# Kernel tuning notes

Hardware: AMD Instinct MI355X
Metric: run time of the kernel (lower is better)

The kernel has to match this reference:

```python
import jax, jax.numpy as jnp
import numpy as np

N_SAMPLES = 32768
SAMPLES_PER_FRAME = 256
N_FRAMES = N_SAMPLES // SAMPLES_PER_FRAME  # 128
SAMPLERATE = 22050
NYQUIST = SAMPLERATE // 2
MIN_FREQ = 40.0 / NYQUIST
MAX_FREQ = 4000.0 / NYQUIST
FREQ_SCALE = MAX_FREQ - MIN_FREQ
TWO_PI = 2.0 * np.pi


def lin_interp(x, out_size):
    """torch F.interpolate(mode='linear', align_corners=False) along last axis."""
    in_size = x.shape[-1]
    scale = in_size / out_size
    coords = (jnp.arange(out_size, dtype=x.dtype) + 0.5) * scale - 0.5
    coords = jnp.clip(coords, 0.0, in_size - 1)
    i0 = jnp.floor(coords).astype(jnp.int32)
    i1 = jnp.minimum(i0 + 1, in_size - 1)
    w = coords - i0.astype(x.dtype)
    return x[..., i0] * (1.0 - w) + x[..., i1] * w


def setup_inputs() -> dict:
    key = jax.random.key(0)
    k1, k2 = jax.random.split(key)
    f0 = jax.random.uniform(k1, (4, 16, 1), dtype=jnp.float32)  # normalized freq in [0,1)
    # resonance decay factors, realistic range near [0.75, 0.999)
    res = 0.75 + 0.249 * jax.random.uniform(k2, (4, 16, 32), dtype=jnp.float32)
    factors = jnp.arange(1, 33, dtype=jnp.float32)  # harmonic multipliers 1..32
    return {"f0": f0, "res": res, "factors": factors}


def reference(f0, res, factors):
    B, E, _ = f0.shape
    F_ = factors.shape[0]
    # map f0 in [0,1] to normalized frequency band
    f0 = MIN_FREQ + FREQ_SCALE * f0                      # (B, E, 1)
    freqs = f0 * factors[None, None, :]                  # (B, E, F)
    freqs = jnp.where(freqs >= 1.0, 0.0, freqs)          # zero out aliased harmonics
    # repeat per frame then upsample to sample rate
    freqs = jnp.broadcast_to(freqs[..., None], (B, E, F_, N_FRAMES))
    freqs = lin_interp(freqs, N_SAMPLES)                 # (B, E, F, N_SAMPLES)
    # exponential decay envelope: cumprod over frames via exp(cumsum(log))
    log_res = jnp.log(res + 1e-12)                       # (B, E, F)
    log_env = jnp.cumsum(
        jnp.broadcast_to(log_res[..., None], (B, E, F_, N_FRAMES)), axis=-1)
    env = jnp.exp(log_env)
    env = lin_interp(env, N_SAMPLES)                     # (B, E, F, N_SAMPLES)
    # integrate phase and oscillate
    phase = jnp.cumsum(freqs * TWO_PI, axis=-1)
    final = env * jnp.sin(phase)                         # (B, E, F, N_SAMPLES)
    return jnp.sum(final, axis=2)                        # (B, E, N_SAMPLES)
```

## Files before the change

### kernel.cpp

```cpp
#include <hip/hip_runtime.h>
#include <hip/hip_bf16.h>


#define NSAMP 32768
#define NFRM  128
#define NF    32
#define NP2   (NF / 2)
#define NPAIR 64
#define CHUNKS 16
#define CHUNK (NSAMP / CHUNKS)
#define KIT   (CHUNK / 256)

typedef __attribute__((ext_vector_type(2))) float f32x2;

__device__ __forceinline__ f32x2 pk_fma(f32x2 a, f32x2 b, f32x2 c) {
    return __builtin_elementwise_fma(a, b, c);
}

__device__ __forceinline__ float ldin(const void* p, int i, bool isbf) {
    if (isbf) {
        unsigned int w = ((unsigned int)((const unsigned short*)p)[i]) << 16;
        float f; __builtin_memcpy(&f, &w, 4); return f;
    }
    return ((const float*)p)[i];
}

__device__ __forceinline__ float rfl(float x) {
    int i; __builtin_memcpy(&i, &x, 4);
    i = __builtin_amdgcn_readfirstlane(i);
    float f; __builtin_memcpy(&f, &i, 4); return f;
}

extern "C" __global__ __launch_bounds__(256, 4)
void reson_kernel(const void* __restrict__ f0p,
                  const void* __restrict__ resp,
                  const void* __restrict__ facp,
                  void* __restrict__ outp)
{
    const bool isbf = (((const unsigned int*)facp)[0] != 0x3F800000u);

    const int pair = blockIdx.x;
    const int y    = blockIdx.y;
    const int tid  = threadIdx.x;
    const int n0   = y * CHUNK + tid;

    const float MINF = (float)(40.0 / 11025.0);
    const float FSC  = (float)(3960.0 / 11025.0);

    __shared__ __align__(16) float sR[NF];
    __shared__ __align__(16) float sP[NF];

    const float f0v = rfl(ldin(f0p, pair, isbf));
    const float sf0 = MINF + FSC * f0v;
    const unsigned int Q1 = (unsigned int)((double)sf0 * 4294967296.0 + 0.5);

    if (tid < NF) {
        const float r   = ldin(resp, pair * NF + tid, isbf);
        const float fac = ldin(facp, tid, isbf);
        float P = exp2f(log2f(r) * (float)(8 * y));
        if (sf0 * fac >= 1.0f) P = 0.0f;
        sR[tid] = r;
        sP[tid] = P;
    }
    __syncthreads();

    const float c0raw = (n0 + 0.5f) * (1.0f / 256.0f) - 0.5f;
    const bool useR1 = (tid >= 128) || (y == 0);

    f32x2 E[NP2];
    f32x2 Rv[NP2];
    #pragma unroll
    for (int j = 0; j < NP2; ++j) {
        const f32x2 p2 = *(const f32x2*)&sP[2 * j];
        const f32x2 r2 = *(const f32x2*)&sR[2 * j];
        Rv[j].x = rfl(r2.x); Rv[j].y = rfl(r2.y);
        E[j] = useR1 ? (f32x2)(p2 * Rv[j]) : p2;
    }

    const int obase = pair * NSAMP + n0;

    if (y != 0 && y != CHUNKS - 1) {
        const float w0 = c0raw - floorf(c0raw);
        const f32x2 w0v = {w0, w0};
        #pragma unroll
        for (int j = 0; j < NP2; ++j) {
            const f32x2 M = E[j];
            E[j] = pk_fma(w0v, pk_fma(M, Rv[j], -M), M);
        }
        #pragma unroll 1
        for (int k = 0; k < KIT; ++k) {
            const unsigned int nn = (unsigned int)(n0 + (k << 8) + 1);
            const unsigned int qn = Q1 * nn;
            const float t1 = (float)qn * 0x1p-32f;
            const float t2 = (float)(qn << 1) * 0x1p-32f;
            const float s1 = __builtin_amdgcn_sinf(t1);
            const float s2 = __builtin_amdgcn_sinf(t2);
            const float c2 = __builtin_amdgcn_cosf(t2);
            const float k2s = c2 + c2;
            const f32x2 k2 = {k2s, k2s};
            f32x2 sp = {-s1, 0.0f};
            f32x2 sc = {s1, s2};
            f32x2 a0 = {0.0f, 0.0f}, a1 = {0.0f, 0.0f};
            #pragma unroll
            for (int j = 0; j < NP2; ++j) {
                if (j & 1) a1 = pk_fma(E[j], sc, a1);
                else       a0 = pk_fma(E[j], sc, a0);
                E[j] = E[j] * Rv[j];
                const f32x2 sn = pk_fma(k2, sc, -sp);
                sp = sc; sc = sn;
            }
            const f32x2 as = a0 + a1;
            const float acc = as.x + as.y;
            const int o = obase + (k << 8);
            if (isbf) ((__hip_bfloat16*)outp)[o] = __float2bfloat16(acc);
            else      ((float*)outp)[o] = acc;
        }
    } else {
        const float c0 = fminf(fmaxf(c0raw, 0.0f), 127.0f);
        const float w0 = c0 - floorf(c0);
        const float c1e = c0raw + 1.0f;
        const float w1 = c1e - floorf(c1e);
        const bool clampLow = (y == 0) && (c0raw < 0.0f);
        #pragma unroll 1
        for (int k = 0; k < KIT; ++k) {
            const unsigned int nn = (unsigned int)(n0 + (k << 8) + 1);
            const unsigned int qn = Q1 * nn;
            const float t1 = (float)qn * 0x1p-32f;
            const float t2 = (float)(qn << 1) * 0x1p-32f;
            const float s1 = __builtin_amdgcn_sinf(t1);
            const float s2 = __builtin_amdgcn_sinf(t2);
            const float c2 = __builtin_amdgcn_cosf(t2);
            const float k2s = c2 + c2;
            const f32x2 k2 = {k2s, k2s};
            f32x2 sp = {-s1, 0.0f};
            f32x2 sc = {s1, s2};
            const float wk = (k == 0)
                ? w0 : ((c0raw + (float)k > 127.0f) ? 0.0f : w1);
            const f32x2 wkv = {wk, wk};
            const bool adv = !((k == 0) && clampLow);
            f32x2 a0 = {0.0f, 0.0f}, a1 = {0.0f, 0.0f};
            #pragma unroll
            for (int j = 0; j < NP2; ++j) {
                const f32x2 M   = E[j];
                const f32x2 An  = M * Rv[j];
                const f32x2 env = pk_fma(wkv, An - M, M);
                if (j & 1) a1 = pk_fma(env, sc, a1);
                else       a0 = pk_fma(env, sc, a0);
                E[j] = adv ? An : M;
                const f32x2 sn = pk_fma(k2, sc, -sp);
                sp = sc; sc = sn;
            }
            const f32x2 as = a0 + a1;
            const float acc = as.x + as.y;
            const int o = obase + (k << 8);
            if (isbf) ((__hip_bfloat16*)outp)[o] = __float2bfloat16(acc);
            else      ((float*)outp)[o] = acc;
        }
    }
}

extern "C" void kernel_launch(void* const* d_in, const int* in_sizes, int n_in,
                              void* d_out, int out_size, void* d_ws, size_t ws_size,
                              hipStream_t stream) {
    (void)in_sizes; (void)n_in; (void)out_size; (void)d_ws; (void)ws_size;
    dim3 grid(NPAIR, CHUNKS);
    dim3 block(256);
    reson_kernel<<<grid, block, 0, stream>>>(d_in[0], d_in[1], d_in[2], d_out);
}
```

Baseline: 67.36 us.

## Double chunk count and replace packed-FMA harmonic recurrence with scalar chain

Splits each pair's samples into 32 chunks instead of 16, halving iterations per thread and doubling grid size, with launch bounds raised to 8 waves per EU. The packed f32x2 two-lane sine recurrence (which needed an extra sin/cos of the doubled phase) becomes a single scalar Chebyshev recurrence over all 32 harmonics from one sin/cos pair. This trades packed-math throughput and a longer serial dependency chain for fewer transcendental ops and more parallel blocks to hide latency. Envelope-start precompute now scales by KIT so the envelope stays correct for the new chunking.

```diff
diff --git a/kernel.cpp b/kernel.cpp
--- a/kernel.cpp
+++ b/kernel.cpp
@@ -5,17 +5,10 @@
 #define NSAMP 32768
 #define NFRM  128
 #define NF    32
-#define NP2   (NF / 2)
 #define NPAIR 64
-#define CHUNKS 16
+#define CHUNKS 32
 #define CHUNK (NSAMP / CHUNKS)
 #define KIT   (CHUNK / 256)
-
-typedef __attribute__((ext_vector_type(2))) float f32x2;
-
-__device__ __forceinline__ f32x2 pk_fma(f32x2 a, f32x2 b, f32x2 c) {
-    return __builtin_elementwise_fma(a, b, c);
-}
 
 __device__ __forceinline__ float ldin(const void* p, int i, bool isbf) {
     if (isbf) {
@@ -31,7 +24,7 @@
     float f; __builtin_memcpy(&f, &i, 4); return f;
 }
 
-extern "C" __global__ __launch_bounds__(256, 4)
+extern "C" __global__ __launch_bounds__(256, 8)
 void reson_kernel(const void* __restrict__ f0p,
                   const void* __restrict__ resp,
                   const void* __restrict__ facp,
@@ -57,7 +50,7 @@
     if (tid < NF) {
         const float r   = ldin(resp, pair * NF + tid, isbf);
         const float fac = ldin(facp, tid, isbf);
-        float P = exp2f(log2f(r) * (float)(8 * y));
+        float P = exp2f(log2f(r) * (float)(KIT * y));
         if (sf0 * fac >= 1.0f) P = 0.0f;
         sR[tid] = r;
         sP[tid] = P;
@@ -67,50 +60,48 @@
     const float c0raw = (n0 + 0.5f) * (1.0f / 256.0f) - 0.5f;
     const bool useR1 = (tid >= 128) || (y == 0);
 
-    f32x2 E[NP2];
-    f32x2 Rv[NP2];
+    float E[NF];
+    float Rg[NF];
     #pragma unroll
-    for (int j = 0; j < NP2; ++j) {
-        const f32x2 p2 = *(const f32x2*)&sP[2 * j];
-        const f32x2 r2 = *(const f32x2*)&sR[2 * j];
-        Rv[j].x = rfl(r2.x); Rv[j].y = rfl(r2.y);
-        E[j] = useR1 ? (f32x2)(p2 * Rv[j]) : p2;
+    for (int f4 = 0; f4 < NF; f4 += 4) {
+        const float4 p4 = *(const float4*)&sP[f4];
+        const float4 r4 = *(const float4*)&sR[f4];
+        Rg[f4+0] = rfl(r4.x); Rg[f4+1] = rfl(r4.y);
+        Rg[f4+2] = rfl(r4.z); Rg[f4+3] = rfl(r4.w);
+        E[f4+0] = useR1 ? p4.x * Rg[f4+0] : p4.x;
+        E[f4+1] = useR1 ? p4.y * Rg[f4+1] : p4.y;
+        E[f4+2] = useR1 ? p4.z * Rg[f4+2] : p4.z;
+        E[f4+3] = useR1 ? p4.w * Rg[f4+3] : p4.w;
     }
 
     const int obase = pair * NSAMP + n0;
 
     if (y != 0 && y != CHUNKS - 1) {
         const float w0 = c0raw - floorf(c0raw);
-        const f32x2 w0v = {w0, w0};
         #pragma unroll
-        for (int j = 0; j < NP2; ++j) {
-            const f32x2 M = E[j];
-            E[j] = pk_fma(w0v, pk_fma(M, Rv[j], -M), M);
+        for (int f = 0; f < NF; ++f) {
+            const float M = E[f];
+            E[f] = fmaf(w0, fmaf(M, Rg[f], -M), M);
         }
         #pragma unroll 1
         for (int k = 0; k < KIT; ++k) {
             const unsigned int nn = (unsigned int)(n0 + (k << 8) + 1);
             const unsigned int qn = Q1 * nn;
-            const float t1 = (float)qn * 0x1p-32f;
-            const float t2 = (float)(qn << 1) * 0x1p-32f;
-            const float s1 = __builtin_amdgcn_sinf(t1);
-            const float s2 = __builtin_amdgcn_sinf(t2);
-            const float c2 = __builtin_amdgcn_cosf(t2);
-            const float k2s = c2 + c2;
-            const f32x2 k2 = {k2s, k2s};
-            f32x2 sp = {-s1, 0.0f};
-            f32x2 sc = {s1, s2};
-            f32x2 a0 = {0.0f, 0.0f}, a1 = {0.0f, 0.0f};
+            const float t  = (float)qn * 0x1p-32f;
+            const float s1 = __builtin_amdgcn_sinf(t);
+            const float c1 = __builtin_amdgcn_cosf(t);
+            const float k2 = c1 + c1;
+            float sp = 0.0f, sc = s1;
+            float a0 = 0.0f, a1 = 0.0f;
             #pragma unroll
-            for (int j = 0; j < NP2; ++j) {
-                if (j & 1) a1 = pk_fma(E[j], sc, a1);
-                else       a0 = pk_fma(E[j], sc, a0);
-                E[j] = E[j] * Rv[j];
-                const f32x2 sn = pk_fma(k2, sc, -sp);
+            for (int f = 0; f < NF; ++f) {
+                if (f & 1) a1 = fmaf(E[f], sc, a1);
+                else       a0 = fmaf(E[f], sc, a0);
+                E[f] *= Rg[f];
+                const float sn = fmaf(k2, sc, -sp);
                 sp = sc; sc = sn;
             }
-            const f32x2 as = a0 + a1;
-            const float acc = as.x + as.y;
+            const float acc = a0 + a1;
             const int o = obase + (k << 8);
             if (isbf) ((__hip_bfloat16*)outp)[o] = __float2bfloat16(acc);
             else      ((float*)outp)[o] = acc;
@@ -125,33 +116,27 @@
         for (int k = 0; k < KIT; ++k) {
             const unsigned int nn = (unsigned int)(n0 + (k << 8) + 1);
             const unsigned int qn = Q1 * nn;
-            const float t1 = (float)qn * 0x1p-32f;
-            const float t2 = (float)(qn << 1) * 0x1p-32f;
-            const float s1 = __builtin_amdgcn_sinf(t1);
-            const float s2 = __builtin_amdgcn_sinf(t2);
-            const float c2 = __builtin_amdgcn_cosf(t2);
-            const float k2s = c2 + c2;
-            const f32x2 k2 = {k2s, k2s};
-            f32x2 sp = {-s1, 0.0f};
-            f32x2 sc = {s1, s2};
+            const float t  = (float)qn * 0x1p-32f;
+            const float s1 = __builtin_amdgcn_sinf(t);
+            const float cc = __builtin_amdgcn_cosf(t);
+            const float k2 = cc + cc;
+            float sp = 0.0f, sc = s1;
             const float wk = (k == 0)
                 ? w0 : ((c0raw + (float)k > 127.0f) ? 0.0f : w1);
-            const f32x2 wkv = {wk, wk};
             const bool adv = !((k == 0) && clampLow);
-            f32x2 a0 = {0.0f, 0.0f}, a1 = {0.0f, 0.0f};
+            float a0 = 0.0f, a1 = 0.0f;
             #pragma unroll
-            for (int j = 0; j < NP2; ++j) {
-                const f32x2 M   = E[j];
-                const f32x2 An  = M * Rv[j];
-                const f32x2 env = pk_fma(wkv, An - M, M);
-                if (j & 1) a1 = pk_fma(env, sc, a1);
-                else       a0 = pk_fma(env, sc, a0);
-                E[j] = adv ? An : M;
-                const f32x2 sn = pk_fma(k2, sc, -sp);
+            for (int f = 0; f < NF; ++f) {
+                const float M   = E[f];
+                const float An  = M * Rg[f];
+                const float env = fmaf(wk, An - M, M);
+                if (f & 1) a1 = fmaf(env, sc, a1);
+                else       a0 = fmaf(env, sc, a0);
+                E[f] = adv ? An : M;
+                const float sn = fmaf(k2, sc, -sp);
                 sp = sc; sc = sn;
             }
-            const f32x2 as = a0 + a1;
-            const float acc = as.x + as.y;
+            const float acc = a0 + a1;
             const int o = obase + (k << 8);
             if (isbf) ((__hip_bfloat16*)outp)[o] = __float2bfloat16(acc);
             else      ((float*)outp)[o] = acc;
```

Result: slower. 73.60 us (+9.3%).
